# Performance work log

Hardware: AMD Instinct MI355X
Metric: run time of the kernel (lower is better)

## Reference

```python
import jax, jax.numpy as jnp
import numpy as np

B, N, M = 2048, 4096, 4096


def setup_inputs() -> dict:
    key = jax.random.key(0)
    kt, kv, kr = jax.random.split(key, 3)
    # sorted abscissae per sample (interp1d assumes monotone t)
    t = jnp.sort(jax.random.uniform(kt, (B, N), dtype=jnp.float32), axis=-1)
    v = jax.random.normal(kv, (B, N), dtype=jnp.float32)
    # queries slightly outside [0,1] to exercise the extrapolation clamp
    r = jax.random.uniform(kr, (B, M), minval=-0.05, maxval=1.05, dtype=jnp.float32)
    return {"t": t, "v": v, "r": r}


def _interp1(t, v, r):
    # t: [N] sorted, v: [N], r: [M]
    idx = jnp.clip(jnp.searchsorted(t, r, side='right'), 1, t.shape[0] - 1)
    t0 = t[idx - 1]
    t1 = t[idx]
    v0 = v[idx - 1]
    v1 = v[idx]
    denom = jnp.where(t1 == t0, jnp.float32(1.0), t1 - t0)
    out = v0 + (r - t0) / denom * (v1 - v0)
    # scipy fill_value=(v[0], v[-1]) with bounds_error=False: clamp extrapolation
    out = jnp.where(r < t[0], v[0], out)
    out = jnp.where(r > t[-1], v[-1], out)
    return out


def reference(t, v, r):
    # batched 1D linear interpolation with clamped extrapolation -> [B, M]
    return jax.vmap(_interp1)(t, v, r)
```

## Files before the change

### kernel.cpp

```cpp
#include <hip/hip_runtime.h>

constexpr int B = 2048;
constexpr int N = 4096;
constexpr int M = 4096;
constexpr int K = 2048;

__global__ __launch_bounds__(256) void interp_kernel(
    const float* __restrict__ t,
    const float* __restrict__ v,
    const float* __restrict__ r,
    float* __restrict__ out) {
    __shared__ float2 stv[N];
    __shared__ int lut[K];

    const int b = blockIdx.x;
    const float* tb = t + (size_t)b * N;
    const float* vb = v + (size_t)b * N;
    const float* rb = r + (size_t)b * M;
    float* ob = out + (size_t)b * M;

    for (int i = threadIdx.x; i < N / 4; i += blockDim.x) {
        const float4 t4 = ((const float4*)tb)[i];
        const float4 v4 = ((const float4*)vb)[i];
        stv[4 * i + 0] = make_float2(t4.x, v4.x);
        stv[4 * i + 1] = make_float2(t4.y, v4.y);
        stv[4 * i + 2] = make_float2(t4.z, v4.z);
        stv[4 * i + 3] = make_float2(t4.w, v4.w);
    }
    for (int k = threadIdx.x; k < K; k += blockDim.x) lut[k] = N;
    __syncthreads();

    for (int j = threadIdx.x; j < N; j += blockDim.x) {
        const float tj = stv[j].x;
        int khi = (int)(tj * K);
        if (khi > K - 1) khi = K - 1;
        int klo = 0;
        if (j > 0) klo = (int)(stv[j - 1].x * K) + 1;
        for (int k = klo; k <= khi; ++k) lut[k] = j;
    }
    __syncthreads();

    const float tfirst = stv[0].x;
    const float vfirst = stv[0].y;
    const float tlast = stv[N - 1].x;
    const float vlast = stv[N - 1].y;

    const float4* r4 = (const float4*)rb;
    float4* o4 = (float4*)ob;
    for (int base = 0; base < M / 4; base += 2 * 256) {
        const int ia = base + threadIdx.x;
        const int ib = ia + 256;
        const float4 qa = r4[ia];
        const float4 qb = r4[ib];
        float q[8] = {qa.x, qa.y, qa.z, qa.w, qb.x, qb.y, qb.z, qb.w};
        int lo[8], hi[8];

        #pragma unroll
        for (int j = 0; j < 8; ++j) {
            int k = (int)(q[j] * K);
            k = k < 0 ? 0 : (k > K - 1 ? K - 1 : k);
            lo[j] = lut[k];
            hi[j] = (k == K - 1) ? N : lut[k + 1];
        }
        #pragma unroll
        for (int j = 0; j < 8; ++j) {
            #pragma unroll
            for (int s = 0; s < 3; ++s) {
                const int safe = lo[j] < N - 1 ? lo[j] : N - 1;
                const bool adv = (lo[j] < hi[j]) && (stv[safe].x <= q[j]);
                lo[j] += adv ? 1 : 0;
            }
            while (lo[j] < hi[j] && stv[lo[j]].x <= q[j]) ++lo[j];
        }
        float o[8];
        #pragma unroll
        for (int j = 0; j < 8; ++j) {
            const int idx = lo[j] < 1 ? 1 : (lo[j] > N - 1 ? N - 1 : lo[j]);
            const float2 p0 = stv[idx - 1];
            const float2 p1 = stv[idx];
            const float denom = (p1.x == p0.x) ? 1.0f : (p1.x - p0.x);
            float oo = p0.y + (q[j] - p0.x) / denom * (p1.y - p0.y);
            oo = (q[j] < tfirst) ? vfirst : oo;
            oo = (q[j] > tlast) ? vlast : oo;
            o[j] = oo;
        }
        o4[ia] = make_float4(o[0], o[1], o[2], o[3]);
        o4[ib] = make_float4(o[4], o[5], o[6], o[7]);
    }
}

extern "C" void kernel_launch(void* const* d_in, const int* in_sizes, int n_in,
                              void* d_out, int out_size, void* d_ws, size_t ws_size,
                              hipStream_t stream) {
    const float* t = (const float*)d_in[0];
    const float* v = (const float*)d_in[1];
    const float* r = (const float*)d_in[2];
    float* out = (float*)d_out;
    interp_kernel<<<B, 256, 0, stream>>>(t, v, r, out);
}
```

Before: 153.2 us.

## Use 512-thread blocks, drop hi bound lookup, and use fast reciprocal

Doubles the block size to 512 threads so each thread handles exactly 8 queries with no outer loop. The search upper bound from the lookup table is replaced by a plain bound at N, which removes one shared load per query. The exact division is replaced with the hardware approximate reciprocal. Larger blocks speed up smem staging and LUT building but may limit how many blocks fit per CU, and the approximate reciprocal can change numerics slightly.

After: 140.8 us. -8.1%, faster.

```diff
diff --git a/kernel.cpp b/kernel.cpp
--- a/kernel.cpp
+++ b/kernel.cpp
@@ -4,8 +4,9 @@
 constexpr int N = 4096;
 constexpr int M = 4096;
 constexpr int K = 2048;
+constexpr int T = 512;
 
-__global__ __launch_bounds__(256) void interp_kernel(
+__global__ __launch_bounds__(T, 8) void interp_kernel(
     const float* __restrict__ t,
     const float* __restrict__ v,
     const float* __restrict__ r,
@@ -19,7 +20,7 @@
     const float* rb = r + (size_t)b * M;
     float* ob = out + (size_t)b * M;
 
-    for (int i = threadIdx.x; i < N / 4; i += blockDim.x) {
+    for (int i = threadIdx.x; i < N / 4; i += T) {
         const float4 t4 = ((const float4*)tb)[i];
         const float4 v4 = ((const float4*)vb)[i];
         stv[4 * i + 0] = make_float2(t4.x, v4.x);
@@ -27,10 +28,10 @@
         stv[4 * i + 2] = make_float2(t4.z, v4.z);
         stv[4 * i + 3] = make_float2(t4.w, v4.w);
     }
-    for (int k = threadIdx.x; k < K; k += blockDim.x) lut[k] = N;
+    for (int k = threadIdx.x; k < K; k += T) lut[k] = N;
     __syncthreads();
 
-    for (int j = threadIdx.x; j < N; j += blockDim.x) {
+    for (int j = threadIdx.x; j < N; j += T) {
         const float tj = stv[j].x;
         int khi = (int)(tj * K);
         if (khi > K - 1) khi = K - 1;
@@ -47,46 +48,43 @@
 
     const float4* r4 = (const float4*)rb;
     float4* o4 = (float4*)ob;
-    for (int base = 0; base < M / 4; base += 2 * 256) {
-        const int ia = base + threadIdx.x;
-        const int ib = ia + 256;
-        const float4 qa = r4[ia];
-        const float4 qb = r4[ib];
-        float q[8] = {qa.x, qa.y, qa.z, qa.w, qb.x, qb.y, qb.z, qb.w};
-        int lo[8], hi[8];
+    const int ia = threadIdx.x;
+    const int ib = ia + T;
+    const float4 qa = r4[ia];
+    const float4 qb = r4[ib];
+    float q[8] = {qa.x, qa.y, qa.z, qa.w, qb.x, qb.y, qb.z, qb.w};
+    int lo[8];
 
+    #pragma unroll
+    for (int j = 0; j < 8; ++j) {
+        int k = (int)(q[j] * K);
+        k = k < 0 ? 0 : (k > K - 1 ? K - 1 : k);
+        lo[j] = lut[k];
+    }
+    #pragma unroll
+    for (int j = 0; j < 8; ++j) {
         #pragma unroll
-        for (int j = 0; j < 8; ++j) {
-            int k = (int)(q[j] * K);
-            k = k < 0 ? 0 : (k > K - 1 ? K - 1 : k);
-            lo[j] = lut[k];
-            hi[j] = (k == K - 1) ? N : lut[k + 1];
+        for (int s = 0; s < 3; ++s) {
+            const int safe = lo[j] < N - 1 ? lo[j] : N - 1;
+            lo[j] += (stv[safe].x <= q[j]) ? 1 : 0;
         }
-        #pragma unroll
-        for (int j = 0; j < 8; ++j) {
-            #pragma unroll
-            for (int s = 0; s < 3; ++s) {
-                const int safe = lo[j] < N - 1 ? lo[j] : N - 1;
-                const bool adv = (lo[j] < hi[j]) && (stv[safe].x <= q[j]);
-                lo[j] += adv ? 1 : 0;
-            }
-            while (lo[j] < hi[j] && stv[lo[j]].x <= q[j]) ++lo[j];
-        }
-        float o[8];
-        #pragma unroll
-        for (int j = 0; j < 8; ++j) {
-            const int idx = lo[j] < 1 ? 1 : (lo[j] > N - 1 ? N - 1 : lo[j]);
-            const float2 p0 = stv[idx - 1];
-            const float2 p1 = stv[idx];
-            const float denom = (p1.x == p0.x) ? 1.0f : (p1.x - p0.x);
-            float oo = p0.y + (q[j] - p0.x) / denom * (p1.y - p0.y);
-            oo = (q[j] < tfirst) ? vfirst : oo;
-            oo = (q[j] > tlast) ? vlast : oo;
-            o[j] = oo;
-        }
-        o4[ia] = make_float4(o[0], o[1], o[2], o[3]);
-        o4[ib] = make_float4(o[4], o[5], o[6], o[7]);
+        while (lo[j] < N && stv[lo[j]].x <= q[j]) ++lo[j];
     }
+    float o[8];
+    #pragma unroll
+    for (int j = 0; j < 8; ++j) {
+        const int idx = lo[j] < 1 ? 1 : (lo[j] > N - 1 ? N - 1 : lo[j]);
+        const float2 p0 = stv[idx - 1];
+        const float2 p1 = stv[idx];
+        const float d = p1.x - p0.x;
+        const float rden = __builtin_amdgcn_rcpf(d == 0.0f ? 1.0f : d);
+        float oo = p0.y + (q[j] - p0.x) * rden * (p1.y - p0.y);
+        oo = (q[j] < tfirst) ? vfirst : oo;
+        oo = (q[j] > tlast) ? vlast : oo;
+        o[j] = oo;
+    }
+    o4[ia] = make_float4(o[0], o[1], o[2], o[3]);
+    o4[ib] = make_float4(o[4], o[5], o[6], o[7]);
 }
 
 extern "C" void kernel_launch(void* const* d_in, const int* in_sizes, int n_in,
@@ -96,5 +94,5 @@
     const float* v = (const float*)d_in[1];
     const float* r = (const float*)d_in[2];
     float* out = (float*)d_out;
-    interp_kernel<<<B, 256, 0, stream>>>(t, v, r, out);
+    interp_kernel<<<B, T, 0, stream>>>(t, v, r, out);
 }
```
